# Performance work log

Hardware: AMD Instinct MI355X
Metric: run time of the kernel (lower is better)

Reference implementation:

```python
import jax, jax.numpy as jnp
import numpy as np

N_NODES = 100000
N_EDGES = 1600000
IN_DIM = 128
HID = 128


def sage_conv(x, src, dst, W_l, W_r, b, num_nodes):
    # PyG SAGEConv (mean aggregation): out = lin_l(mean_{j in N(i)} x_j) + lin_r(x_i)
    msgs = x[src]                                            # [E, F] gather
    agg = jax.ops.segment_sum(msgs, dst, num_segments=num_nodes)  # [N, F]
    cnt = jax.ops.segment_sum(jnp.ones((src.shape[0],), x.dtype), dst,
                              num_segments=num_nodes)        # [N]
    agg = agg / jnp.maximum(cnt, 1.0)[:, None]               # mean; 0 for isolated nodes
    return agg @ W_l + b + x @ W_r


def setup_inputs() -> dict:
    key = jax.random.key(0)
    ks = jax.random.split(key, 12)
    s_in = 1.0 / np.sqrt(IN_DIM)
    s_h = 1.0 / np.sqrt(HID)
    return {
        "x": jax.random.normal(ks[0], (N_NODES, IN_DIM), jnp.float32),
        "edge_index": jax.random.randint(ks[1], (2, N_EDGES), 0, N_NODES, jnp.int64),
        "Wl1": jax.random.normal(ks[2], (IN_DIM, HID), jnp.float32) * s_in,
        "Wr1": jax.random.normal(ks[3], (IN_DIM, HID), jnp.float32) * s_in,
        "b1": jnp.zeros((HID,), jnp.float32),
        "Wl2": jax.random.normal(ks[4], (HID, HID), jnp.float32) * s_h,
        "Wr2": jax.random.normal(ks[5], (HID, HID), jnp.float32) * s_h,
        "b2": jnp.zeros((HID,), jnp.float32),
        "Wp": jax.random.normal(ks[6], (HID, 1), jnp.float32) * s_h,
        "bp": jnp.zeros((1,), jnp.float32),
        "Wd": jax.random.normal(ks[7], (HID, 1), jnp.float32) * s_h,
        "bd": jnp.zeros((1,), jnp.float32),
    }


def reference(x, edge_index, Wl1, Wr1, b1, Wl2, Wr2, b2, Wp, bp, Wd, bd):
    src, dst = edge_index[0], edge_index[1]
    h = jax.nn.relu(sage_conv(x, src, dst, Wl1, Wr1, b1, N_NODES))
    h = jax.nn.relu(sage_conv(h, src, dst, Wl2, Wr2, b2, N_NODES))
    preds = h @ Wp + bp                      # [N, 1]
    diffs = jax.nn.sigmoid(h @ Wd + bd)      # [N, 1]
    return (preds - diffs, preds + diffs)
```

## Files before the change

kernel.cpp:

```cpp
#include <hip/hip_runtime.h>
#include <hip/hip_bf16.h>

#define N_NODES 100000
#define N_EDGES 1600000
#define NBUCK 1563
#define BCAP 1216
#define PADC 1408
#define ACHUNK 4096
#define GTILES 1563

typedef __bf16 bf16x8 __attribute__((ext_vector_type(8)));
typedef __bf16 bf16x4 __attribute__((ext_vector_type(4)));
typedef float  f32x4  __attribute__((ext_vector_type(4)));
typedef float  f32x2  __attribute__((ext_vector_type(2)));


#define ACCV(v)                                              \
  a01 += __builtin_amdgcn_cvt_pk_f32_fp8((v).x, false);      \
  a23 += __builtin_amdgcn_cvt_pk_f32_fp8((v).x, true);       \
  a45 += __builtin_amdgcn_cvt_pk_f32_fp8((v).y, false);      \
  a67 += __builtin_amdgcn_cvt_pk_f32_fp8((v).y, true);


__global__ __launch_bounds__(256) void init_kernel(int* __restrict__ bcnt,
                                                   int* __restrict__ P1s,
                                                   int* __restrict__ P2s,
                                                   const float* __restrict__ Wl1,
                                                   const float* __restrict__ Wr1,
                                                   const float* __restrict__ Wl2,
                                                   const float* __restrict__ Wr2,
                                                   __bf16* __restrict__ W1out,
                                                   __bf16* __restrict__ W2out) {
  const int b = blockIdx.x, t = threadIdx.x;
  if (b == 0) {
    for (int i = t; i < NBUCK; i += 256) bcnt[i] = 0;
    if (t < 32) { P1s[t] = 0; P2s[t] = 0; }
    return;
  }
  int gi = (b - 1) * 256 + t;
  bool L2 = gi >= 32768;
  int i = gi & 32767;
  int j = i & 7;
  int lane = (i >> 3) & 63;
  int c = (i >> 9) & 3;
  int tile = i >> 11;
  int k = c * 32 + ((lane >> 4) * 8) + j;
  int krow = L2 ? (((k & 7) << 4) | (k >> 3)) : k;
  int col = tile * 16 + (lane & 15);
  const float* Wl = L2 ? Wl2 : Wl1;
  const float* Wr = L2 ? Wr2 : Wr1;
  float v = (col < 128) ? Wl[krow * 128 + col] : Wr[krow * 128 + (col - 128)];
  (L2 ? W2out : W1out)[i] = (__bf16)v;
}


__global__ __launch_bounds__(256, 4) void work1_kernel(
    const float* __restrict__ A, const __bf16* __restrict__ Wswz,
    const float* __restrict__ bias, unsigned char* __restrict__ P,
    __bf16* __restrict__ R, int M,
    const int* __restrict__ src, const int* __restrict__ dst,
    int* __restrict__ bcnt, unsigned* __restrict__ packed, int E) {
  __shared__ __align__(16) char smem[64 * 144 * 2];
  const int t = threadIdx.x;

  if (blockIdx.x >= GTILES) {
    int* hist = (int*)smem;
    int* curs = (int*)(smem + 6272);
    for (int i = t; i < NBUCK; i += 256) hist[i] = 0;
    __syncthreads();

    const int base = (blockIdx.x - GTILES) * ACHUNK;
    const int lim = min(base + ACHUNK, E);

    int dloc[16], sloc[16];
    int myn = 0;
    for (int i = base + t; i < lim; i += 256) {
      dloc[myn] = dst[i];
      sloc[myn] = src[i];
      ++myn;
    }
    for (int k = 0; k < myn; ++k) atomicAdd(&hist[dloc[k] >> 6], 1);
    __syncthreads();

    for (int i = t; i < NBUCK; i += 256) {
      int h = hist[i];
      curs[i] = (h > 0) ? atomicAdd(&bcnt[i], h) : 0;
    }
    __syncthreads();

    for (int k = 0; k < myn; ++k) {
      int d = dloc[k];
      int b = d >> 6;
      int pos = atomicAdd(&curs[b], 1);
      if (pos < BCAP)
        packed[(size_t)b * BCAP + pos] = ((unsigned)sloc[k] << 6) | (unsigned)(d & 63);
    }
    return;
  }

  __bf16 (*ldsA)[144] = (__bf16 (*)[144])smem;
  const int lane = t & 63;
  const int w = t >> 6;
  const int q = lane >> 4;
  const int s = lane & 15;
  const int m0 = blockIdx.x * 64;

#pragma unroll
  for (int it = 0; it < 8; ++it) {
    int row = it * 8 + (t >> 5);
    int col = (t & 31) * 4;
    float4 v = make_float4(0.f, 0.f, 0.f, 0.f);
    if (m0 + row < M) v = *(const float4*)&A[(size_t)(m0 + row) * 128 + col];
    bf16x4 bv;
    bv.x = (__bf16)v.x; bv.y = (__bf16)v.y; bv.z = (__bf16)v.z; bv.w = (__bf16)v.w;
    *(bf16x4*)&ldsA[row][col] = bv;
  }

  float breg[4];
#pragma unroll
  for (int j = 0; j < 4; ++j)
    breg[j] = (w >= 2) ? bias[((w - 2) * 4 + j) * 16 + s] : 0.f;

  __syncthreads();

#pragma unroll
  for (int half = 0; half < 2; ++half) {
    f32x4 acc[8];
    f32x4 zero = {0.f, 0.f, 0.f, 0.f};
#pragma unroll
    for (int i = 0; i < 8; ++i) acc[i] = zero;

#pragma unroll
    for (int c = 0; c < 4; ++c) {
      bf16x8 a0 = *(const bf16x8*)&ldsA[(half * 2 + 0) * 16 + s][c * 32 + q * 8];
      bf16x8 a1 = *(const bf16x8*)&ldsA[(half * 2 + 1) * 16 + s][c * 32 + q * 8];
#pragma unroll
      for (int ct = 0; ct < 4; ++ct) {
        bf16x8 b = *(const bf16x8*)&Wswz[(size_t)((((w * 4 + ct) * 4 + c) * 64) + lane) * 8];
        acc[ct]     = __builtin_amdgcn_mfma_f32_16x16x32_bf16(a0, b, acc[ct], 0, 0, 0);
        acc[4 + ct] = __builtin_amdgcn_mfma_f32_16x16x32_bf16(a1, b, acc[4 + ct], 0, 0, 0);
      }
    }

#pragma unroll
    for (int i = 0; i < 2; ++i) {
      int rt = half * 2 + i;
#pragma unroll
      for (int r = 0; r < 4; ++r) {
        int row = m0 + rt * 16 + q * 4 + r;
        if (row < M) {
          if (w < 2) {
            unsigned v = 0;
            v = __builtin_amdgcn_cvt_pk_fp8_f32(acc[i * 4 + 0][r], acc[i * 4 + 1][r], v, false);
            v = __builtin_amdgcn_cvt_pk_fp8_f32(acc[i * 4 + 2][r], acc[i * 4 + 3][r], v, true);
            *(unsigned*)&P[(size_t)row * 128 + s * 8 + w * 4] = v;
          } else {
            bf16x4 o;
#pragma unroll
            for (int ct = 0; ct < 4; ++ct) o[ct] = (__bf16)(acc[i * 4 + ct][r] + breg[ct]);
            *(bf16x4*)&R[(size_t)row * 128 + s * 8 + (w - 2) * 4] = o;
          }
        }
      }
    }
  }
}


__global__ __launch_bounds__(256, 6) void fusedB_kernel(
    const unsigned char* __restrict__ P1, __bf16* R,
    const unsigned* __restrict__ pck, const int* __restrict__ bcnt,
    const __bf16* __restrict__ Wswz, const float* __restrict__ bias,
    unsigned char* __restrict__ P2, int N) {
  __shared__ __bf16 Hlds[64][144];
  __shared__ int ssrcL[PADC];
  __shared__ int hist[64], pexcl[64], curs[64], scanb[64];
  __shared__ int gsteal;
  const int t = threadIdx.x;
  const int lane = t & 63;
  const int w = t >> 6;
  const int q = lane >> 4;
  const int s = lane & 15;
  const int b = blockIdx.x, nb = b * 64;

  if (t < 64) hist[t] = 0;
  if (t == 0) gsteal = 0;
  __syncthreads();

  const int ecnt = min(bcnt[b], BCAP);
  const unsigned* pk = pck + (size_t)b * BCAP;
  unsigned ploc[5];
  int myn = 0;
  for (int i = t; i < ecnt; i += 256) {
    unsigned p = pk[i];
    ploc[myn++] = p;
    atomicAdd(&hist[p & 63u], 1);
  }
  __syncthreads();

  int c0 = (t < 64) ? hist[t] : 0;
  int pc = (c0 + 3) & ~3;
  int x = pc;
  if (t < 64) scanb[t] = x;
  __syncthreads();
  for (int d = 1; d < 64; d <<= 1) {
    int y = (t >= d && t < 64) ? scanb[t - d] : 0;
    __syncthreads();
    if (t < 64) { x += y; scanb[t] = x; }
    __syncthreads();
  }
  if (t < 64) { pexcl[t] = x - pc; curs[t] = x - pc; }
  __syncthreads();

  for (int k = 0; k < myn; ++k) {
    unsigned p = ploc[k];
    int r = atomicAdd(&curs[p & 63u], 1);
    ssrcL[r] = (int)(p >> 6);
  }
  if (t < 64)
    for (int j = c0; j < pc; ++j) ssrcL[pexcl[t] + j] = N;
  __syncthreads();

  const unsigned char* Pb = P1 + (size_t)s * 8;
  for (;;) {
    int n4;
    if (lane == 0) n4 = atomicAdd(&gsteal, 4);
    n4 = __shfl(n4, 0, 64);
    if (n4 >= 64) break;
    int dl = n4 + q;
    int node = nb + dl;
    int start = pexcl[dl];
    int dg = hist[dl];
    int pend = start + ((dg + 3) & ~3);

    f32x2 a01 = {0.f, 0.f}, a23 = {0.f, 0.f}, a45 = {0.f, 0.f}, a67 = {0.f, 0.f};
    int cur = start;
    for (; cur + 8 <= pend; cur += 8) {
      int4 sv0 = *(const int4*)&ssrcL[cur];
      int4 sv1 = *(const int4*)&ssrcL[cur + 4];
      uint2 v0 = *(const uint2*)(Pb + (size_t)sv0.x * 128);
      uint2 v1 = *(const uint2*)(Pb + (size_t)sv0.y * 128);
      uint2 v2 = *(const uint2*)(Pb + (size_t)sv0.z * 128);
      uint2 v3 = *(const uint2*)(Pb + (size_t)sv0.w * 128);
      uint2 v4 = *(const uint2*)(Pb + (size_t)sv1.x * 128);
      uint2 v5 = *(const uint2*)(Pb + (size_t)sv1.y * 128);
      uint2 v6 = *(const uint2*)(Pb + (size_t)sv1.z * 128);
      uint2 v7 = *(const uint2*)(Pb + (size_t)sv1.w * 128);
      ACCV(v0) ACCV(v1) ACCV(v2) ACCV(v3)
      ACCV(v4) ACCV(v5) ACCV(v6) ACCV(v7)
    }
    if (cur < pend) {
      int4 sv = *(const int4*)&ssrcL[cur];
      uint2 v0 = *(const uint2*)(Pb + (size_t)sv.x * 128);
      uint2 v1 = *(const uint2*)(Pb + (size_t)sv.y * 128);
      uint2 v2 = *(const uint2*)(Pb + (size_t)sv.z * 128);
      uint2 v3 = *(const uint2*)(Pb + (size_t)sv.w * 128);
      ACCV(v0) ACCV(v1) ACCV(v2) ACCV(v3)
    }

    int nc = min(node, N - 1);
    float inv = 1.0f / (float)(dg > 0 ? dg : 1);
    bf16x8 rv = *(const bf16x8*)&R[(size_t)nc * 128 + s * 8];
    float acc1[8] = {a01[0], a01[1], a23[0], a23[1], a45[0], a45[1], a67[0], a67[1]};
    bf16x8 hh;
#pragma unroll
    for (int j = 0; j < 8; ++j)
      hh[j] = (__bf16)fmaxf(acc1[j] * inv + (float)rv[j], 0.f);
    *(bf16x8*)&Hlds[dl][s * 8] = hh;
  }
  __syncthreads();

  float breg[4];
#pragma unroll
  for (int j = 0; j < 4; ++j)
    breg[j] = (w >= 2) ? bias[((w - 2) * 4 + j) * 16 + s] : 0.f;

#pragma unroll
  for (int half = 0; half < 2; ++half) {
    f32x4 acc[8];
    f32x4 zero = {0.f, 0.f, 0.f, 0.f};
#pragma unroll
    for (int i = 0; i < 8; ++i) acc[i] = zero;

#pragma unroll
    for (int c = 0; c < 4; ++c) {
      bf16x8 a0 = *(const bf16x8*)&Hlds[(half * 2 + 0) * 16 + s][c * 32 + q * 8];
      bf16x8 a1 = *(const bf16x8*)&Hlds[(half * 2 + 1) * 16 + s][c * 32 + q * 8];
#pragma unroll
      for (int ct = 0; ct < 4; ++ct) {
        bf16x8 b = *(const bf16x8*)&Wswz[(size_t)((((w * 4 + ct) * 4 + c) * 64) + lane) * 8];
        acc[ct]     = __builtin_amdgcn_mfma_f32_16x16x32_bf16(a0, b, acc[ct], 0, 0, 0);
        acc[4 + ct] = __builtin_amdgcn_mfma_f32_16x16x32_bf16(a1, b, acc[4 + ct], 0, 0, 0);
      }
    }

#pragma unroll
    for (int i = 0; i < 2; ++i) {
      int rt = half * 2 + i;
#pragma unroll
      for (int r = 0; r < 4; ++r) {
        int row = nb + rt * 16 + q * 4 + r;
        if (row < N) {
          if (w < 2) {
            unsigned v = 0;
            v = __builtin_amdgcn_cvt_pk_fp8_f32(acc[i * 4 + 0][r], acc[i * 4 + 1][r], v, false);
            v = __builtin_amdgcn_cvt_pk_fp8_f32(acc[i * 4 + 2][r], acc[i * 4 + 3][r], v, true);
            *(unsigned*)&P2[(size_t)row * 128 + s * 8 + w * 4] = v;
          } else {
            bf16x4 o;
#pragma unroll
            for (int ct = 0; ct < 4; ++ct) o[ct] = (__bf16)(acc[i * 4 + ct][r] + breg[ct]);
            *(bf16x4*)&R[(size_t)row * 128 + s * 8 + (w - 2) * 4] = o;
          }
        }
      }
    }
  }
}


__global__ __launch_bounds__(256, 6) void fusedC_kernel(
    const unsigned char* __restrict__ P2, const __bf16* __restrict__ R,
    const unsigned* __restrict__ pck, const int* __restrict__ bcnt,
    float* __restrict__ out,
    const float* __restrict__ Wp, const float* __restrict__ Wd,
    const float* __restrict__ bp, const float* __restrict__ bd, int N) {
  __shared__ int ssrcL[PADC];
  __shared__ int hist[64], pexcl[64], curs[64], scanb[64];
  __shared__ int gsteal;
  const int t = threadIdx.x;
  const int lane = t & 63;
  const int q = lane >> 4;
  const int s = lane & 15;
  const int b = blockIdx.x, nb = b * 64;

  if (t < 64) hist[t] = 0;
  if (t == 0) gsteal = 0;
  __syncthreads();

  const int ecnt = min(bcnt[b], BCAP);
  const unsigned* pk = pck + (size_t)b * BCAP;
  unsigned ploc[5];
  int myn = 0;
  for (int i = t; i < ecnt; i += 256) {
    unsigned p = pk[i];
    ploc[myn++] = p;
    atomicAdd(&hist[p & 63u], 1);
  }
  __syncthreads();

  int c0 = (t < 64) ? hist[t] : 0;
  int pc = (c0 + 3) & ~3;
  int x = pc;
  if (t < 64) scanb[t] = x;
  __syncthreads();
  for (int d = 1; d < 64; d <<= 1) {
    int y = (t >= d && t < 64) ? scanb[t - d] : 0;
    __syncthreads();
    if (t < 64) { x += y; scanb[t] = x; }
    __syncthreads();
  }
  if (t < 64) { pexcl[t] = x - pc; curs[t] = x - pc; }
  __syncthreads();

  for (int k = 0; k < myn; ++k) {
    unsigned p = ploc[k];
    int r = atomicAdd(&curs[p & 63u], 1);
    ssrcL[r] = (int)(p >> 6);
  }
  if (t < 64)
    for (int j = c0; j < pc; ++j) ssrcL[pexcl[t] + j] = N;
  __syncthreads();

  const unsigned char* Pb = P2 + (size_t)s * 8;
  for (;;) {
    int n4;
    if (lane == 0) n4 = atomicAdd(&gsteal, 4);
    n4 = __shfl(n4, 0, 64);
    if (n4 >= 64) break;
    int dl = n4 + q;
    int node = nb + dl;
    int start = pexcl[dl];
    int dg = hist[dl];
    int pend = start + ((dg + 3) & ~3);

    f32x2 a01 = {0.f, 0.f}, a23 = {0.f, 0.f}, a45 = {0.f, 0.f}, a67 = {0.f, 0.f};
    int cur = start;
    for (; cur + 8 <= pend; cur += 8) {
      int4 sv0 = *(const int4*)&ssrcL[cur];
      int4 sv1 = *(const int4*)&ssrcL[cur + 4];
      uint2 v0 = *(const uint2*)(Pb + (size_t)sv0.x * 128);
      uint2 v1 = *(const uint2*)(Pb + (size_t)sv0.y * 128);
      uint2 v2 = *(const uint2*)(Pb + (size_t)sv0.z * 128);
      uint2 v3 = *(const uint2*)(Pb + (size_t)sv0.w * 128);
      uint2 v4 = *(const uint2*)(Pb + (size_t)sv1.x * 128);
      uint2 v5 = *(const uint2*)(Pb + (size_t)sv1.y * 128);
      uint2 v6 = *(const uint2*)(Pb + (size_t)sv1.z * 128);
      uint2 v7 = *(const uint2*)(Pb + (size_t)sv1.w * 128);
      ACCV(v0) ACCV(v1) ACCV(v2) ACCV(v3)
      ACCV(v4) ACCV(v5) ACCV(v6) ACCV(v7)
    }
    if (cur < pend) {
      int4 sv = *(const int4*)&ssrcL[cur];
      uint2 v0 = *(const uint2*)(Pb + (size_t)sv.x * 128);
      uint2 v1 = *(const uint2*)(Pb + (size_t)sv.y * 128);
      uint2 v2 = *(const uint2*)(Pb + (size_t)sv.z * 128);
      uint2 v3 = *(const uint2*)(Pb + (size_t)sv.w * 128);
      ACCV(v0) ACCV(v1) ACCV(v2) ACCV(v3)
    }

    int nc = min(node, N - 1);
    float inv = 1.0f / (float)(dg > 0 ? dg : 1);
    bf16x8 rv = *(const bf16x8*)&R[(size_t)nc * 128 + s * 8];
    float acc[8] = {a01[0], a01[1], a23[0], a23[1], a45[0], a45[1], a67[0], a67[1]};
    float p = 0.f, dd = 0.f;
#pragma unroll
    for (int j = 0; j < 8; ++j) {
      float h = fmaxf(acc[j] * inv + (float)rv[j], 0.f);
      p += h * Wp[j * 16 + s];
      dd += h * Wd[j * 16 + s];
    }
    p += __shfl_xor(p, 1, 64);  p += __shfl_xor(p, 2, 64);
    p += __shfl_xor(p, 4, 64);  p += __shfl_xor(p, 8, 64);
    dd += __shfl_xor(dd, 1, 64); dd += __shfl_xor(dd, 2, 64);
    dd += __shfl_xor(dd, 4, 64); dd += __shfl_xor(dd, 8, 64);
    if (node < N && s == 0) {
      float preds = p + bp[0];
      float sg = 1.0f / (1.0f + __expf(-(dd + bd[0])));
      out[node] = preds - sg;
      out[N + node] = preds + sg;
    }
  }
}


extern "C" void kernel_launch(void* const* d_in, const int* in_sizes, int n_in,
                              void* d_out, int out_size, void* d_ws, size_t ws_size,
                              hipStream_t stream) {
  const float* x    = (const float*)d_in[0];
  const int*   ei   = (const int*)d_in[1];
  const float* Wl1 = (const float*)d_in[2];
  const float* Wr1 = (const float*)d_in[3];
  const float* b1  = (const float*)d_in[4];
  const float* Wl2 = (const float*)d_in[5];
  const float* Wr2 = (const float*)d_in[6];
  const float* b2  = (const float*)d_in[7];
  const float* Wp  = (const float*)d_in[8];
  const float* bp  = (const float*)d_in[9];
  const float* Wd  = (const float*)d_in[10];
  const float* bd  = (const float*)d_in[11];
  float* out = (float*)d_out;

  const int N = N_NODES, E = N_EDGES;
  const int* src = ei;
  const int* dst = ei + E;

  char* w = (char*)d_ws;
  unsigned char* P1 = (unsigned char*)w; w += (size_t)(N + 1) * 128;
  unsigned char* P2 = (unsigned char*)w; w += (size_t)(N + 1) * 128;
  __bf16* Rbuf   = (__bf16*)w;   w += (size_t)N * 128 * 2;
  unsigned* pck  = (unsigned*)w; w += (size_t)NBUCK * BCAP * 4;
  int* bcnt      = (int*)w;      w += (size_t)(NBUCK + 32) * 4;
  __bf16* Ws1    = (__bf16*)w;   w += 65536;
  __bf16* Ws2    = (__bf16*)w;   w += 65536;

  const int PABLK = (E + ACHUNK - 1) / ACHUNK;

  init_kernel<<<257, 256, 0, stream>>>(bcnt,
                                       (int*)(P1 + (size_t)N * 128),
                                       (int*)(P2 + (size_t)N * 128),
                                       Wl1, Wr1, Wl2, Wr2, Ws1, Ws2);
  work1_kernel<<<GTILES + PABLK, 256, 0, stream>>>(x, Ws1, b1, P1, Rbuf, N,
                                                   src, dst, bcnt, pck, E);
  fusedB_kernel<<<NBUCK, 256, 0, stream>>>(P1, Rbuf, pck, bcnt, Ws2, b2, P2, N);
  fusedC_kernel<<<NBUCK, 256, 0, stream>>>(P2, Rbuf, pck, bcnt, out,
                                           Wp, Wd, bp, bd, N);
}
```

Baseline: 271.3 us.

## Reuse per-bucket sorted edge lists from layer-two kernel in final kernel

The layer-two kernel now writes its per-bucket, destination-sorted source list and per-node offset/degree metadata to global memory. The final kernel reads them back instead of redoing the histogram, prefix scan and LDS scatter. The edge-partition blocks are moved to the front of the first kernel's grid so bucketing starts earlier. Occupancy hints for both fused kernels drop from 6 to 4 waves, and the extra global write/read of about 9 MB is traded against the removed atomics and barriers.

```diff
diff --git a/kernel.cpp b/kernel.cpp
--- a/kernel.cpp
+++ b/kernel.cpp
@@ -8,6 +8,7 @@
 #define PADC 1408
 #define ACHUNK 4096
 #define GTILES 1563
+#define PABLK 391
 
 typedef __bf16 bf16x8 __attribute__((ext_vector_type(8)));
 typedef __bf16 bf16x4 __attribute__((ext_vector_type(4)));
@@ -63,13 +64,13 @@
   __shared__ __align__(16) char smem[64 * 144 * 2];
   const int t = threadIdx.x;
 
-  if (blockIdx.x >= GTILES) {
+  if (blockIdx.x < PABLK) {
     int* hist = (int*)smem;
     int* curs = (int*)(smem + 6272);
     for (int i = t; i < NBUCK; i += 256) hist[i] = 0;
     __syncthreads();
 
-    const int base = (blockIdx.x - GTILES) * ACHUNK;
+    const int base = blockIdx.x * ACHUNK;
     const int lim = min(base + ACHUNK, E);
 
     int dloc[16], sloc[16];
@@ -103,7 +104,7 @@
   const int w = t >> 6;
   const int q = lane >> 4;
   const int s = lane & 15;
-  const int m0 = blockIdx.x * 64;
+  const int m0 = (blockIdx.x - PABLK) * 64;
 
 #pragma unroll
   for (int it = 0; it < 8; ++it) {
@@ -167,11 +168,12 @@
 }
 
 
-__global__ __launch_bounds__(256, 6) void fusedB_kernel(
+__global__ __launch_bounds__(256, 4) void fusedB_kernel(
     const unsigned char* __restrict__ P1, __bf16* R,
     const unsigned* __restrict__ pck, const int* __restrict__ bcnt,
     const __bf16* __restrict__ Wswz, const float* __restrict__ bias,
-    unsigned char* __restrict__ P2, int N) {
+    unsigned char* __restrict__ P2, int* __restrict__ srt,
+    int* __restrict__ meta, int N) {
   __shared__ __bf16 Hlds[64][144];
   __shared__ int ssrcL[PADC];
   __shared__ int hist[64], pexcl[64], curs[64], scanb[64];
@@ -220,6 +222,9 @@
   if (t < 64)
     for (int j = c0; j < pc; ++j) ssrcL[pexcl[t] + j] = N;
   __syncthreads();
+
+  for (int i = t; i < PADC; i += 256) srt[(size_t)b * PADC + i] = ssrcL[i];
+  if (t < 64) meta[b * 64 + t] = (pexcl[t] << 16) | hist[t];
 
   const unsigned char* Pb = P1 + (size_t)s * 8;
   for (;;) {
@@ -319,14 +324,14 @@
 }
 
 
-__global__ __launch_bounds__(256, 6) void fusedC_kernel(
+__global__ __launch_bounds__(256, 4) void fusedC_kernel(
     const unsigned char* __restrict__ P2, const __bf16* __restrict__ R,
-    const unsigned* __restrict__ pck, const int* __restrict__ bcnt,
+    const int* __restrict__ srt, const int* __restrict__ meta,
     float* __restrict__ out,
     const float* __restrict__ Wp, const float* __restrict__ Wd,
     const float* __restrict__ bp, const float* __restrict__ bd, int N) {
   __shared__ int ssrcL[PADC];
-  __shared__ int hist[64], pexcl[64], curs[64], scanb[64];
+  __shared__ int hist[64], pexcl[64];
   __shared__ int gsteal;
   const int t = threadIdx.x;
   const int lane = t & 63;
@@ -334,42 +339,13 @@
   const int s = lane & 15;
   const int b = blockIdx.x, nb = b * 64;
 
-  if (t < 64) hist[t] = 0;
+  for (int i = t; i < PADC; i += 256) ssrcL[i] = srt[(size_t)b * PADC + i];
+  if (t < 64) {
+    int m = meta[b * 64 + t];
+    pexcl[t] = m >> 16;
+    hist[t] = m & 0xffff;
+  }
   if (t == 0) gsteal = 0;
-  __syncthreads();
-
-  const int ecnt = min(bcnt[b], BCAP);
-  const unsigned* pk = pck + (size_t)b * BCAP;
-  unsigned ploc[5];
-  int myn = 0;
-  for (int i = t; i < ecnt; i += 256) {
-    unsigned p = pk[i];
-    ploc[myn++] = p;
-    atomicAdd(&hist[p & 63u], 1);
-  }
-  __syncthreads();
-
-  int c0 = (t < 64) ? hist[t] : 0;
-  int pc = (c0 + 3) & ~3;
-  int x = pc;
-  if (t < 64) scanb[t] = x;
-  __syncthreads();
-  for (int d = 1; d < 64; d <<= 1) {
-    int y = (t >= d && t < 64) ? scanb[t - d] : 0;
-    __syncthreads();
-    if (t < 64) { x += y; scanb[t] = x; }
-    __syncthreads();
-  }
-  if (t < 64) { pexcl[t] = x - pc; curs[t] = x - pc; }
-  __syncthreads();
-
-  for (int k = 0; k < myn; ++k) {
-    unsigned p = ploc[k];
-    int r = atomicAdd(&curs[p & 63u], 1);
-    ssrcL[r] = (int)(p >> 6);
-  }
-  if (t < 64)
-    for (int j = c0; j < pc; ++j) ssrcL[pexcl[t] + j] = N;
   __syncthreads();
 
   const unsigned char* Pb = P2 + (size_t)s * 8;
@@ -463,8 +439,8 @@
   int* bcnt      = (int*)w;      w += (size_t)(NBUCK + 32) * 4;
   __bf16* Ws1    = (__bf16*)w;   w += 65536;
   __bf16* Ws2    = (__bf16*)w;   w += 65536;
-
-  const int PABLK = (E + ACHUNK - 1) / ACHUNK;
+  int* srt       = (int*)w;      w += (size_t)NBUCK * PADC * 4;
+  int* meta      = (int*)w;      w += (size_t)NBUCK * 64 * 4;
 
   init_kernel<<<257, 256, 0, stream>>>(bcnt,
                                        (int*)(P1 + (size_t)N * 128),
@@ -472,7 +448,8 @@
                                        Wl1, Wr1, Wl2, Wr2, Ws1, Ws2);
   work1_kernel<<<GTILES + PABLK, 256, 0, stream>>>(x, Ws1, b1, P1, Rbuf, N,
                                                    src, dst, bcnt, pck, E);
-  fusedB_kernel<<<NBUCK, 256, 0, stream>>>(P1, Rbuf, pck, bcnt, Ws2, b2, P2, N);
-  fusedC_kernel<<<NBUCK, 256, 0, stream>>>(P2, Rbuf, pck, bcnt, out,
+  fusedB_kernel<<<NBUCK, 256, 0, stream>>>(P1, Rbuf, pck, bcnt, Ws2, b2, P2,
+                                           srt, meta, N);
+  fusedC_kernel<<<NBUCK, 256, 0, stream>>>(P2, Rbuf, srt, meta, out,
                                            Wp, Wd, bp, bd, N);
 }
```

Result: faster. 227.1 us (-16.3%).
